# Performance work log

Measured on AMD Instinct MI355X. Metric: run time of the kernel, lower is better.

Reference implementation:

```python
import jax, jax.numpy as jnp
import numpy as np

D = 384; QK = 48; E = 768; LOCAL = E - D
NB = 8; NTOK = 100; NEG = -1e30
B = 128; S = 100; NPTS = 256


def layernorm(x, w, eps=1e-5):
    mu = jnp.mean(x, axis=-1, keepdims=True)
    var = jnp.mean((x - mu) ** 2, axis=-1, keepdims=True)
    return (x - mu) * jax.lax.rsqrt(var + eps) * w


def attend(q, k, v, bias=None):
    scale = 1.0 / jnp.sqrt(jnp.asarray(q.shape[-1], q.dtype))
    s = jnp.einsum('bqd,bkd->bqk', q, k) * scale
    if bias is not None:
        s = s + bias
    return jnp.einsum('bqk,bkd->bqd', jax.nn.softmax(s, axis=-1), v)


def setup_inputs() -> dict:
    key = jax.random.key(0)
    ks = jax.random.split(key, 16)
    s_exp = 0.5 / (D ** 0.5) / 2.0   # 0.5 / sqrt(residual_depth) / expand_factor
    s_prj = 1.0 / (D ** 0.5) / 2.0 / NB
    return {
        'q': jax.random.randint(ks[0], (B, S), 0, NTOK),
        'pts': jax.random.randint(ks[1], (B, NPTS, 2), 0, NTOK),
        'emb': jax.random.normal(ks[2], (NTOK, D), jnp.float32),
        'pt_emb': jax.random.normal(ks[3], (NTOK, D // 2), jnp.float32),
        'norm_w': jnp.ones((D,), jnp.float32),
        'out_w': jax.random.normal(ks[4], (NTOK, D), jnp.float32) / (D ** 0.5),
        'ln1': jnp.ones((NB, D), jnp.float32),
        'expand': s_exp * jax.random.normal(ks[5], (NB, 2 * QK + 2 * E, D), jnp.float32),
        'project1': s_prj * jax.random.normal(ks[6], (NB, D, E), jnp.float32),
        'bias_mult': jnp.ones((NB,), jnp.float32),
        'ln2': jnp.ones((NB, D), jnp.float32),
        'Wq': s_exp * jax.random.normal(ks[7], (NB, QK + 2 * LOCAL, D), jnp.float32),
        'Wkv': s_exp * jax.random.normal(ks[8], (NB, QK + 2 * D, D), jnp.float32),
        'project2': s_prj * jax.random.normal(ks[9], (NB, D, E), jnp.float32),
    }


def _forward(q, pts, emb, pt_emb, norm_w, out_w, ln1, expand, project1, bias_mult, ln2, Wq, Wkv, project2):
    x = emb[q]                                        # [B,S,D]
    kv = pt_emb[pts].reshape(pts.shape[0], -1, D)     # [B,NPTS,D] (pairs of 2D coords fold into D)
    x = layernorm(x, norm_w)

    pos = jnp.arange(x.shape[1])
    pbb = (pos[None, :] - pos[:, None]).astype(x.dtype)  # position bias base (j - i)
    allowed = pos[None, :] <= pos[:, None]                # causal: attend to past + self

    def step(h, p):
        w_ln1, W_e, W_p1, bm, w_ln2, W_q, W_kv, W_p2 = p
        # --- latent self-attention block ---
        bias = jnp.where(allowed, jax.nn.softplus(bm) * pbb, NEG)
        n = layernorm(h, w_ln1)
        proj = n @ W_e.T                                  # [B,S,2*QK+2*E]
        qr = proj[..., :QK]
        kr = proj[..., QK:2 * QK]
        lin = proj[..., 2 * QK:2 * QK + E]
        pre = proj[..., 2 * QK + E:]
        geglu = lin * jax.nn.gelu(pre, approximate=False)
        attn = attend(qr, kr, geglu[..., LOCAL:], bias)
        h = h + jnp.concatenate([geglu[..., :LOCAL], attn], axis=-1) @ W_p1.T
        # --- latent cross-attention block ---
        n = layernorm(h, w_ln2)
        pq = n @ W_q.T                                    # [B,S,QK+2*LOCAL]
        qr2 = pq[..., :QK]
        g_local = pq[..., QK:QK + LOCAL] * jax.nn.gelu(pq[..., QK + LOCAL:], approximate=False)
        pk = kv @ W_kv.T                                  # [B,NPTS,QK+2*D]
        k2 = pk[..., :QK]
        g_val = pk[..., QK:QK + D] * jax.nn.gelu(pk[..., QK + D:], approximate=False)
        attn2 = attend(qr2, k2, g_val)
        h = h + jnp.concatenate([g_local, attn2], axis=-1) @ W_p2.T
        return h, None

    x, _ = jax.lax.scan(step, x, (ln1, expand, project1, bias_mult, ln2, Wq, Wkv, project2))
    x = layernorm(x, norm_w)
    return x @ out_w.T                                    # [B,S,NTOK]


def reference(q, pts, emb, pt_emb, norm_w, out_w, ln1, expand, project1, bias_mult, ln2, Wq, Wkv, project2):
    return _forward(q, pts, emb, pt_emb, norm_w, out_w, ln1, expand, project1, bias_mult, ln2, Wq, Wkv, project2)
```

## Files before the change

kernel.cpp:

```cpp
#include <hip/hip_runtime.h>
#include <hip/hip_bf16.h>
#include <math.h>

#define B_    128
#define S_    100
#define D_    384
#define QK_   48
#define E_    768
#define LOCAL_ 384
#define NB_   8
#define NTOK_ 100
#define NPTS_ 256
#define M_    (B_*S_)

typedef unsigned short ushort;
typedef __attribute__((ext_vector_type(8))) short  bf16x8;
typedef __attribute__((ext_vector_type(8))) unsigned short ushort8v;
typedef __attribute__((ext_vector_type(4))) float  f32x4;

#define MFMA(a,b,c) __builtin_amdgcn_mfma_f32_16x16x32_bf16(a,b,c,0,0,0)

static __device__ __forceinline__ float gelu_f(float x) {
    float y = 1.5957691216057308f * (x + 0.044715f * x * x * x);
    float e = __expf(y);
    float t = 1.0f - 2.0f / (e + 1.0f);
    return 0.5f * x * (1.0f + t);
}
static __device__ __forceinline__ ushort f2b(float f) {
    union { float f; unsigned u; } x; x.f = f;
    unsigned r = x.u + 0x7FFFu + ((x.u >> 16) & 1u);
    return (ushort)(r >> 16);
}
static __device__ __forceinline__ float b2f(ushort u) {
    union { unsigned u; float f; } x; x.u = ((unsigned)u) << 16;
    return x.f;
}

static __device__ __forceinline__ void xcd_swz(int xn, int gy, int& bx, int& by) {
    int L = blockIdx.x + xn * blockIdx.y;
    int gmain = (gy & ~7) * xn;
    if (L < gmain) {
        int grp = L / (8 * xn);
        int r = L % (8 * xn);
        bx = r >> 3;
        by = grp * 8 + (r & 7);
    } else {
        int Lp = L - gmain;
        int tail = gy & 7;
        by = (gy & ~7) + (Lp % tail);
        bx = Lp / tail;
    }
}

__global__ __launch_bounds__(256)
void ln_rows(const float* __restrict__ X, const float* __restrict__ w,
             ushort* __restrict__ Y, int nrows)
{
    int row = blockIdx.x * 4 + (threadIdx.x >> 6);
    if (row >= nrows) return;
    int lane = threadIdx.x & 63;
    const float* x = X + (size_t)row * D_;
    float v[6]; float s = 0.f;
    #pragma unroll
    for (int t = 0; t < 6; ++t) { v[t] = x[lane + 64*t]; s += v[t]; }
    #pragma unroll
    for (int off = 32; off; off >>= 1) s += __shfl_xor(s, off);
    float mu = s * (1.f/(float)D_);
    float q = 0.f;
    #pragma unroll
    for (int t = 0; t < 6; ++t) { float d = v[t]-mu; q += d*d; }
    #pragma unroll
    for (int off = 32; off; off >>= 1) q += __shfl_xor(q, off);
    float rs = rsqrtf(q * (1.f/(float)D_) + 1e-5f);
    #pragma unroll
    for (int t = 0; t < 6; ++t)
        Y[(size_t)row*D_ + lane + 64*t] = f2b((v[t]-mu)*rs*w[lane + 64*t]);
}

__global__ __launch_bounds__(256)
void x_init(const int* __restrict__ qtok, const float* __restrict__ emb,
            const float* __restrict__ w, float* __restrict__ Y, int nrows)
{
    int row = blockIdx.x * 4 + (threadIdx.x >> 6);
    if (row >= nrows) return;
    int lane = threadIdx.x & 63;
    const float* x = emb + (size_t)qtok[row] * D_;
    float v[6]; float s = 0.f;
    #pragma unroll
    for (int t = 0; t < 6; ++t) { v[t] = x[lane + 64*t]; s += v[t]; }
    #pragma unroll
    for (int off = 32; off; off >>= 1) s += __shfl_xor(s, off);
    float mu = s * (1.f/(float)D_);
    float q = 0.f;
    #pragma unroll
    for (int t = 0; t < 6; ++t) { float d = v[t]-mu; q += d*d; }
    #pragma unroll
    for (int off = 32; off; off >>= 1) q += __shfl_xor(q, off);
    float rs = rsqrtf(q * (1.f/(float)D_) + 1e-5f);
    float* y = Y + (size_t)row * D_;
    #pragma unroll
    for (int t = 0; t < 6; ++t) y[lane + 64*t] = (v[t]-mu)*rs*w[lane + 64*t];
}

#define WE_SZ  (1632*384)
#define P1_SZ  (384*768)
#define WQ_SZ  (816*384)
#define P2_SZ  (384*768)
#define WTOT   (WE_SZ + P1_SZ + WQ_SZ + P2_SZ)

static __device__ __forceinline__ void wsplit(float v, ushort* wh, ushort* wl, size_t o) {
    ushort h = f2b(v);
    wh[o] = h; wl[o] = f2b(v - b2f(h));
}

__global__ __launch_bounds__(256)
void wconv_all_hi(const float* __restrict__ expand, const float* __restrict__ proj1,
                  const float* __restrict__ wq, const float* __restrict__ proj2,
                  ushort* __restrict__ wh)
{
    int i = blockIdx.x*256 + threadIdx.x;
    if (i >= WTOT) return;
    int blk = blockIdx.y;
    float v;
    if (i < WE_SZ) v = expand[(size_t)blk*WE_SZ + i];
    else if (i < WE_SZ+P1_SZ) v = proj1[(size_t)blk*P1_SZ + (i - WE_SZ)];
    else if (i < WE_SZ+P1_SZ+WQ_SZ) v = wq[(size_t)blk*WQ_SZ + (i - WE_SZ - P1_SZ)];
    else v = proj2[(size_t)blk*P2_SZ + (i - WE_SZ - P1_SZ - WQ_SZ)];
    wh[(size_t)blk*WTOT + i] = f2b(v);
}

__global__ __launch_bounds__(256)
void wconv_hi(const float* __restrict__ we, const float* __restrict__ p1,
              const float* __restrict__ wq, const float* __restrict__ p2,
              ushort* __restrict__ wh)
{
    int i = blockIdx.x*256 + threadIdx.x;
    if (i >= WTOT) return;
    float v;
    if (i < WE_SZ) v = we[i];
    else if (i < WE_SZ+P1_SZ) v = p1[i - WE_SZ];
    else if (i < WE_SZ+P1_SZ+WQ_SZ) v = wq[i - WE_SZ - P1_SZ];
    else v = p2[i - WE_SZ - P1_SZ - WQ_SZ];
    wh[i] = f2b(v);
}

__global__ __launch_bounds__(256)
void wconv1(const float* __restrict__ src, int n,
            ushort* __restrict__ wh, ushort* __restrict__ wl)
{
    int i = blockIdx.x*256 + threadIdx.x;
    if (i >= n) return;
    wsplit(src[i], wh, wl, i);
}

__global__ __launch_bounds__(256)
void pconv(const float* __restrict__ src, ushort* __restrict__ dst)
{
    int i = blockIdx.x*256 + threadIdx.x;
    if (i >= 128*192) return;
    int r = i / 192;
    dst[i] = (r < NTOK_) ? f2b(src[i]) : 0;
}

__global__ __launch_bounds__(256)
void mm_bt64(const ushort* __restrict__ A1, int lda1, int K1,
             const ushort* __restrict__ A2, int lda2,
             const ushort* __restrict__ Wgh, const ushort* __restrict__ Wgl,
             float* __restrict__ C, int ldc, int N, int K, int accum)
{
    __shared__ ushort Ah[64][72], Wh[64][72], Wl[64][72];
    int tid = threadIdx.x;
    int row0 = blockIdx.y*64, col0 = blockIdx.x*64;
    int srow = tid >> 3;
    int sseg = (tid & 7) * 8;
    int wid = tid >> 6, lane = tid & 63;
    int wr = wid >> 1, wc = wid & 1;
    int fr = lane & 15, fg = lane >> 4;
    f32x4 acc[2][2] = {};
    for (int k0 = 0; k0 < K; k0 += 64) {
        ushort8v va[2], vc[2], vd[2];
        #pragma unroll
        for (int p = 0; p < 2; ++p) {
            int r = p*32 + srow;
            int arow = row0 + r;
            int wrow = col0 + r;
            int gk = k0 + sseg;
            if (gk < K1) va[p] = *(const ushort8v*)(A1 + (size_t)arow*lda1 + gk);
            else         va[p] = *(const ushort8v*)(A2 + (size_t)arow*lda2 + (gk-K1));
            if (wrow >= N) wrow = N - 1;
            vc[p] = *(const ushort8v*)(Wgh + (size_t)wrow*K + gk);
            vd[p] = *(const ushort8v*)(Wgl + (size_t)wrow*K + gk);
        }
        __syncthreads();
        #pragma unroll
        for (int p = 0; p < 2; ++p) {
            int r = p*32 + srow;
            *(ushort8v*)&Ah[r][sseg] = va[p];
            *(ushort8v*)&Wh[r][sseg] = vc[p];
            *(ushort8v*)&Wl[r][sseg] = vd[p];
        }
        __syncthreads();
        #pragma unroll
        for (int kk = 0; kk < 64; kk += 32) {
            bf16x8 a[2], b_h[2], b_l[2];
            #pragma unroll
            for (int s = 0; s < 2; ++s) {
                a[s]   = *(const bf16x8*)&Ah[wr*32 + s*16 + fr][kk + fg*8];
                b_h[s] = *(const bf16x8*)&Wh[wc*32 + s*16 + fr][kk + fg*8];
                b_l[s] = *(const bf16x8*)&Wl[wc*32 + s*16 + fr][kk + fg*8];
            }
            #pragma unroll
            for (int s = 0; s < 2; ++s)
                #pragma unroll
                for (int u = 0; u < 2; ++u)
                    acc[s][u] = MFMA(a[s], b_h[u], acc[s][u]);
            #pragma unroll
            for (int s = 0; s < 2; ++s)
                #pragma unroll
                for (int u = 0; u < 2; ++u)
                    acc[s][u] = MFMA(a[s], b_l[u], acc[s][u]);
        }
        __syncthreads();
    }
    #pragma unroll
    for (int s = 0; s < 2; ++s) {
        int r = row0 + wr*32 + s*16 + fg*4;
        #pragma unroll
        for (int u = 0; u < 2; ++u) {
            int c = col0 + wc*32 + u*16 + fr;
            if (c < N) {
                #pragma unroll
                for (int j = 0; j < 4; ++j) {
                    size_t o = (size_t)(r+j)*ldc + c;
                    C[o] = accum ? (C[o] + acc[s][u][j]) : acc[s][u][j];
                }
            }
        }
    }
}

__global__ __launch_bounds__(256)
void mm_bt2(const ushort* __restrict__ A1, int lda1, int K1,
            const ushort* __restrict__ A2, int lda2,
            const ushort* __restrict__ Wgh,
            float* __restrict__ C, int ldc, int N, int K, int accum)
{
    __shared__ ushort As[128*32], Whs[64*32];
    int tid = threadIdx.x;
    int lane = tid & 63, wid = tid >> 6;
    int bx, by; xcd_swz(gridDim.x, gridDim.y, bx, by);
    int row0 = by*128, col0 = bx*64;
    int wr = wid >> 1, wc = wid & 1;
    int fr = lane & 15, fg = lane >> 4;
    int gsl = (fg ^ ((fr >> 1) & 3)) * 8;
    int sr = tid >> 2, sg0 = tid & 3;
    int g = sg0 ^ ((sr >> 1) & 3);
    int wrow = col0 + sr; if (wrow >= N) wrow = N - 1;

    ushort8v va[2], vh;
    auto loadk = [&](int k0) {
        const ushort* Asrc; int lda, kk;
        if (k0 < K1) { Asrc = A1; lda = lda1; kk = k0; }
        else         { Asrc = A2; lda = lda2; kk = k0 - K1; }
        #pragma unroll
        for (int i = 0; i < 2; ++i)
            va[i] = *(const ushort8v*)(Asrc + (size_t)(row0 + sr + i*64)*lda + kk + g*8);
        vh = *(const ushort8v*)(Wgh + (size_t)wrow*K + k0 + g*8);
    };

    f32x4 acc[4][2] = {};
    loadk(0);
    for (int k0 = 0; k0 < K; k0 += 32) {
        __syncthreads();
        #pragma unroll
        for (int i = 0; i < 2; ++i)
            *(ushort8v*)&As[(sr + i*64)*32 + sg0*8] = va[i];
        *(ushort8v*)&Whs[sr*32 + sg0*8] = vh;
        if (k0 + 32 < K) loadk(k0 + 32);
        __syncthreads();
        bf16x8 a[4], bh[2];
        #pragma unroll
        for (int s = 0; s < 4; ++s) {
            int r = wr*64 + s*16 + fr;
            a[s] = *(const bf16x8*)&As[r*32 + gsl];
        }
        #pragma unroll
        for (int u = 0; u < 2; ++u) {
            int r = wc*32 + u*16 + fr;
            bh[u] = *(const bf16x8*)&Whs[r*32 + gsl];
        }
        #pragma unroll
        for (int s = 0; s < 4; ++s)
            #pragma unroll
            for (int u = 0; u < 2; ++u)
                acc[s][u] = MFMA(a[s], bh[u], acc[s][u]);
    }
    #pragma unroll
    for (int s = 0; s < 4; ++s) {
        int rb = row0 + wr*64 + s*16 + fg*4;
        #pragma unroll
        for (int u = 0; u < 2; ++u) {
            int c = col0 + wc*32 + u*16 + fr;
            if (c < N) {
                #pragma unroll
                for (int j = 0; j < 4; ++j) {
                    size_t o = (size_t)(rb+j)*ldc + c;
                    C[o] = accum ? (C[o] + acc[s][u][j]) : acc[s][u][j];
                }
            }
        }
    }
}

__global__ __launch_bounds__(256)
void mm_fused2(const ushort* __restrict__ Ag, int lda,
               const ushort* __restrict__ Wqh,
               int Nq, int nqt, float* __restrict__ Qout, int ldq,
               const ushort* __restrict__ W1h, const ushort* __restrict__ W2h,
               ushort* __restrict__ Oh, int ldo, int K)
{
    __shared__ ushort As[128*32];
    __shared__ ushort Xs[2][64*32];
    int tid = threadIdx.x;
    int lane = tid & 63, wid = tid >> 6;
    int bx, by; xcd_swz(gridDim.x, gridDim.y, bx, by);
    int row0 = by*128;
    int wr = wid >> 1, wc = wid & 1;
    int fr = lane & 15, fg = lane >> 4;
    int gsl = (fg ^ ((fr >> 1) & 3)) * 8;
    int sr = tid >> 2, sg0 = tid & 3;
    int g = sg0 ^ ((sr >> 1) & 3);

    if (bx < nqt) {
        int col0 = bx*64;
        int wrow = col0 + sr; if (wrow >= Nq) wrow = Nq - 1;
        ushort8v va[2], vh;
        auto loadk = [&](int k0) {
            #pragma unroll
            for (int i = 0; i < 2; ++i)
                va[i] = *(const ushort8v*)(Ag + (size_t)(row0 + sr + i*64)*lda + k0 + g*8);
            vh = *(const ushort8v*)(Wqh + (size_t)wrow*K + k0 + g*8);
        };
        f32x4 acc[4][2] = {};
        loadk(0);
        for (int k0 = 0; k0 < K; k0 += 32) {
            __syncthreads();
            #pragma unroll
            for (int i = 0; i < 2; ++i)
                *(ushort8v*)&As[(sr + i*64)*32 + sg0*8] = va[i];
            *(ushort8v*)&Xs[0][sr*32 + sg0*8] = vh;
            if (k0 + 32 < K) loadk(k0 + 32);
            __syncthreads();
            bf16x8 a[4], bh[2];
            #pragma unroll
            for (int s = 0; s < 4; ++s) {
                int r = wr*64 + s*16 + fr;
                a[s] = *(const bf16x8*)&As[r*32 + gsl];
            }
            #pragma unroll
            for (int u = 0; u < 2; ++u) {
                int r = wc*32 + u*16 + fr;
                bh[u] = *(const bf16x8*)&Xs[0][r*32 + gsl];
            }
            #pragma unroll
            for (int s = 0; s < 4; ++s)
                #pragma unroll
                for (int u = 0; u < 2; ++u)
                    acc[s][u] = MFMA(a[s], bh[u], acc[s][u]);
        }
        #pragma unroll
        for (int s = 0; s < 4; ++s) {
            int rb = row0 + wr*64 + s*16 + fg*4;
            #pragma unroll
            for (int u = 0; u < 2; ++u) {
                int c = col0 + wc*32 + u*16 + fr;
                if (c < Nq) {
                    #pragma unroll
                    for (int j = 0; j < 4; ++j)
                        Qout[(size_t)(rb+j)*ldq + c] = acc[s][u][j];
                }
            }
        }
    } else {
        int col0 = (bx - nqt)*64;
        ushort8v va[2], vw0, vw2;
        auto loadk = [&](int k0) {
            #pragma unroll
            for (int i = 0; i < 2; ++i)
                va[i] = *(const ushort8v*)(Ag + (size_t)(row0 + sr + i*64)*lda + k0 + g*8);
            size_t wro = (size_t)(col0 + sr)*K + k0 + g*8;
            vw0 = *(const ushort8v*)(W1h + wro);
            vw2 = *(const ushort8v*)(W2h + wro);
        };
        f32x4 acc1[4][2] = {}, acc2[4][2] = {};
        loadk(0);
        for (int k0 = 0; k0 < K; k0 += 32) {
            __syncthreads();
            #pragma unroll
            for (int i = 0; i < 2; ++i)
                *(ushort8v*)&As[(sr + i*64)*32 + sg0*8] = va[i];
            {
                int o = sr*32 + sg0*8;
                *(ushort8v*)&Xs[0][o] = vw0;
                *(ushort8v*)&Xs[1][o] = vw2;
            }
            if (k0 + 32 < K) loadk(k0 + 32);
            __syncthreads();
            bf16x8 a[4], b1[2], b2[2];
            #pragma unroll
            for (int s = 0; s < 4; ++s) {
                int r = wr*64 + s*16 + fr;
                a[s] = *(const bf16x8*)&As[r*32 + gsl];
            }
            #pragma unroll
            for (int u = 0; u < 2; ++u) {
                int r = wc*32 + u*16 + fr;
                b1[u] = *(const bf16x8*)&Xs[0][r*32 + gsl];
                b2[u] = *(const bf16x8*)&Xs[1][r*32 + gsl];
            }
            #pragma unroll
            for (int s = 0; s < 4; ++s)
                #pragma unroll
                for (int u = 0; u < 2; ++u) {
                    acc1[s][u] = MFMA(a[s], b1[u], acc1[s][u]);
                    acc2[s][u] = MFMA(a[s], b2[u], acc2[s][u]);
                }
        }
        #pragma unroll
        for (int s = 0; s < 4; ++s) {
            int rb = row0 + wr*64 + s*16 + fg*4;
            #pragma unroll
            for (int u = 0; u < 2; ++u) {
                int c = col0 + wc*32 + u*16 + fr;
                #pragma unroll
                for (int j = 0; j < 4; ++j) {
                    float gg = acc1[s][u][j] * gelu_f(acc2[s][u][j]);
                    Oh[(size_t)(rb+j)*ldo + c] = f2b(gg);
                }
            }
        }
    }
}

__global__ __launch_bounds__(256)
void pk_mm(const ushort* __restrict__ A,
           const ushort* __restrict__ Wh_, const ushort* __restrict__ Wl_,
           float* __restrict__ P12)
{
    __shared__ ushort Ah[64][72], Wh[64][72], Wl[64][72];
    int tid = threadIdx.x;
    int z = blockIdx.z, blk = z >> 1, half = z & 1;
    int row0 = blockIdx.y*64, col0 = blockIdx.x*64;
    int srow = tid >> 3, sseg = (tid & 7) * 8;
    int wid = tid >> 6, lane = tid & 63;
    int wr = wid >> 1, wc = wid & 1;
    int fr = lane & 15, fg = lane >> 4;
    const ushort* Wbh = Wh_ + (size_t)blk*816*384 + half*192;
    const ushort* Wbl = Wl_ + (size_t)blk*816*384 + half*192;
    float* C = P12 + (size_t)z*128*816;
    f32x4 acc[2][2] = {};
    for (int k0 = 0; k0 < 192; k0 += 64) {
        ushort8v va[2], vc[2], vd[2];
        #pragma unroll
        for (int p = 0; p < 2; ++p) {
            int r = p*32 + srow;
            int wrow = col0 + r; if (wrow >= 816) wrow = 815;
            int gk = k0 + sseg;
            va[p] = *(const ushort8v*)(A + (size_t)(row0 + r)*192 + gk);
            vc[p] = *(const ushort8v*)(Wbh + (size_t)wrow*384 + gk);
            vd[p] = *(const ushort8v*)(Wbl + (size_t)wrow*384 + gk);
        }
        __syncthreads();
        #pragma unroll
        for (int p = 0; p < 2; ++p) {
            int r = p*32 + srow;
            *(ushort8v*)&Ah[r][sseg] = va[p];
            *(ushort8v*)&Wh[r][sseg] = vc[p];
            *(ushort8v*)&Wl[r][sseg] = vd[p];
        }
        __syncthreads();
        #pragma unroll
        for (int kk = 0; kk < 64; kk += 32) {
            bf16x8 a[2], b_h[2], b_l[2];
            #pragma unroll
            for (int s = 0; s < 2; ++s) {
                a[s]   = *(const bf16x8*)&Ah[wr*32 + s*16 + fr][kk + fg*8];
                b_h[s] = *(const bf16x8*)&Wh[wc*32 + s*16 + fr][kk + fg*8];
                b_l[s] = *(const bf16x8*)&Wl[wc*32 + s*16 + fr][kk + fg*8];
            }
            #pragma unroll
            for (int s = 0; s < 2; ++s)
                #pragma unroll
                for (int u = 0; u < 2; ++u)
                    acc[s][u] = MFMA(a[s], b_h[u], acc[s][u]);
            #pragma unroll
            for (int s = 0; s < 2; ++s)
                #pragma unroll
                for (int u = 0; u < 2; ++u)
                    acc[s][u] = MFMA(a[s], b_l[u], acc[s][u]);
        }
        __syncthreads();
    }
    #pragma unroll
    for (int s = 0; s < 2; ++s) {
        int r = row0 + wr*32 + s*16 + fg*4;
        #pragma unroll
        for (int u = 0; u < 2; ++u) {
            int c = col0 + wc*32 + u*16 + fr;
            if (c < 816) {
                #pragma unroll
                for (int j = 0; j < 4; ++j)
                    C[(size_t)(r+j)*816 + c] = acc[s][u][j];
            }
        }
    }
}

template<int NK, int CAUSAL>
__global__ __launch_bounds__(256)
void pv_fused(const float* __restrict__ Q, int ldq,
              const float* __restrict__ Kf, int ldk, int koff, long sK,
              const ushort* __restrict__ V, int ldv, long sV,
              ushort* __restrict__ Oh, int ldo, long sO,
              int Mrows, int Kv,
              const float* __restrict__ bm, int blk)
{
    constexpr int NKF = NK / 16;
    constexpr int PSTR = NK + 8;
    __shared__ ushort SH[64*72 + NK*72];
    __shared__ ushort Vs[128*32];
    ushort* Qs = SH;
    ushort* Ks = SH + 64*72;
    ushort* Pf = SH;

    int L = blockIdx.x + gridDim.x*(blockIdx.y + gridDim.y*blockIdx.z);
    int gz = gridDim.z;
    int zz = L % gz;
    int rest = L / gz;
    int bx = rest % gridDim.x;
    int byy = rest / gridDim.x;
    int row0 = byy*64, col0 = bx*128;

    int tid = threadIdx.x;
    int wv = tid >> 6, lane = tid & 63;
    int fr = lane & 15, fg = lane >> 4;

    const float scale = 0.14433756729740643f;
    float sp = 0.f;
    if (CAUSAL) { float bmv = bm[blk]; sp = (bmv > 20.f) ? bmv : log1pf(expf(bmv)); }

    const float* Qb = Q + ((size_t)zz * S_) * ldq;
    for (int idx = tid; idx < 64*64; idx += 256) {
        int r = idx >> 6, c = idx & 63;
        int grow = row0 + r; if (grow >= S_) grow = S_ - 1;
        ushort v = 0;
        if (c < 48) v = f2b(Qb[(size_t)grow*ldq + c]);
        Qs[r*72 + c] = v;
    }
    const float* Kb = Kf + (size_t)zz*sK + koff;
    for (int idx = tid; idx < NK*64; idx += 256) {
        int j = idx >> 6, c = idx & 63;
        ushort v = 0;
        if (c < 48 && j < Kv) v = f2b(Kb[(size_t)j*ldk + c]);
        Ks[j*72 + c] = v;
    }
    int vk = tid & 31, vcb = (tid >> 5)*8;
    ushort8v vv[2];
    auto loadV = [&](int k0) {
        vv[0] = (ushort8v){0,0,0,0,0,0,0,0};
        vv[1] = (ushort8v){0,0,0,0,0,0,0,0};
        int gk = k0 + vk;
        if (gk < Kv) {
            const ushort* Vb = V + (size_t)zz*sV;
            #pragma unroll
            for (int i2 = 0; i2 < 2; ++i2)
                vv[i2] = *(const ushort8v*)(Vb + (size_t)gk*ldv + col0 + vcb + i2*64);
        }
    };
    loadV(0);
    __syncthreads();

    f32x4 sacc[NKF];
    #pragma unroll
    for (int kf = 0; kf < NKF; ++kf) sacc[kf] = (f32x4){0.f,0.f,0.f,0.f};
    bf16x8 aq0 = *(const bf16x8*)&Qs[(wv*16 + fr)*72 +  0 + fg*8];
    bf16x8 aq1 = *(const bf16x8*)&Qs[(wv*16 + fr)*72 + 32 + fg*8];
    #pragma unroll
    for (int kf = 0; kf < NKF; ++kf) {
        bf16x8 bk0 = *(const bf16x8*)&Ks[(kf*16 + fr)*72 +  0 + fg*8];
        bf16x8 bk1 = *(const bf16x8*)&Ks[(kf*16 + fr)*72 + 32 + fg*8];
        sacc[kf] = MFMA(aq0, bk0, sacc[kf]);
        sacc[kf] = MFMA(aq1, bk1, sacc[kf]);
    }
    #pragma unroll
    for (int j = 0; j < 4; ++j) {
        int i = row0 + wv*16 + fg*4 + j;
        float m = -1e30f;
        #pragma unroll
        for (int kf = 0; kf < NKF; ++kf) {
            int key = kf*16 + fr;
            float s = sacc[kf][j] * scale;
            if (CAUSAL) s = (key <= i) ? (s + sp*(float)(key - i)) : -1e30f;
            sacc[kf][j] = s;
            m = fmaxf(m, s);
        }
        #pragma unroll
        for (int off = 1; off < 16; off <<= 1) m = fmaxf(m, __shfl_xor(m, off));
        float sum = 0.f;
        #pragma unroll
        for (int kf = 0; kf < NKF; ++kf) {
            float p = __expf(sacc[kf][j] - m);
            sacc[kf][j] = p;
            sum += p;
        }
        #pragma unroll
        for (int off = 1; off < 16; off <<= 1) sum += __shfl_xor(sum, off);
        float inv = 1.f / sum;
        #pragma unroll
        for (int kf = 0; kf < NKF; ++kf) sacc[kf][j] *= inv;
    }
    __syncthreads();
    #pragma unroll
    for (int j = 0; j < 4; ++j)
        #pragma unroll
        for (int kf = 0; kf < NKF; ++kf)
            Pf[(wv*16 + fg*4 + j)*PSTR + kf*16 + fr] = f2b(sacc[kf][j]);
    __syncthreads();

    f32x4 acc[4][2] = {};
    for (int k0 = 0; k0 < NK; k0 += 32) {
        #pragma unroll
        for (int i2 = 0; i2 < 2; ++i2) {
            #pragma unroll
            for (int e = 0; e < 8; ++e) {
                int c = vcb + i2*64 + e;
                Vs[c*32 + (vk & 7) + 8*((vk >> 3) ^ ((c >> 3) & 3))] = vv[i2][e];
            }
        }
        if (k0 + 32 < NK) loadV(k0 + 32);
        __syncthreads();
        bf16x8 a[4], b[2];
        #pragma unroll
        for (int s = 0; s < 4; ++s)
            a[s] = *(const bf16x8*)&Pf[(s*16 + fr)*PSTR + k0 + fg*8];
        #pragma unroll
        for (int u = 0; u < 2; ++u) {
            int c = wv*32 + u*16 + fr;
            b[u] = *(const bf16x8*)&Vs[c*32 + 8*(fg ^ ((c >> 3) & 3))];
        }
        #pragma unroll
        for (int s = 0; s < 4; ++s)
            #pragma unroll
            for (int u = 0; u < 2; ++u)
                acc[s][u] = MFMA(a[s], b[u], acc[s][u]);
        __syncthreads();
    }
    ushort* Ohb = Oh + (size_t)zz*sO;
    #pragma unroll
    for (int s = 0; s < 4; ++s) {
        int rbase = row0 + s*16 + fg*4;
        #pragma unroll
        for (int u = 0; u < 2; ++u) {
            int c = col0 + wv*32 + u*16 + fr;
            #pragma unroll
            for (int j = 0; j < 4; ++j) {
                int r = rbase + j;
                if (r < Mrows)
                    Ohb[(size_t)r*ldo + c] = f2b(acc[s][u][j]);
            }
        }
    }
}

__global__ __launch_bounds__(256)
void pk_gather(const int* __restrict__ pts, const float* __restrict__ P12, int blk,
               float* __restrict__ k2, ushort* __restrict__ gv)
{
    int pair = blockIdx.x*4 + (threadIdx.x >> 6);
    int lane = threadIdx.x & 63;
    const float* P1 = P12 + (size_t)(blk*2 + 0)*128*816;
    const float* P2 = P12 + (size_t)(blk*2 + 1)*128*816;
    int t0 = pts[2*pair], t1 = pts[2*pair+1];
    const float* a = P1 + (size_t)t0*816;
    const float* c = P2 + (size_t)t1*816;
    if (lane < QK_) k2[(size_t)pair*QK_ + lane] = a[lane] + c[lane];
    #pragma unroll
    for (int t = 0; t < 6; ++t) {
        int i = lane + 64*t;
        float lin = a[48 + i] + c[48 + i];
        float pre = a[432 + i] + c[432 + i];
        gv[(size_t)pair*D_ + i] = f2b(lin * gelu_f(pre));
    }
}

extern "C" void kernel_launch(void* const* d_in, const int* in_sizes, int n_in,
                              void* d_out, int out_size, void* d_ws, size_t ws_size,
                              hipStream_t stream)
{
    const int*   qtok  = (const int*)d_in[0];
    const int*   pts   = (const int*)d_in[1];
    const float* emb   = (const float*)d_in[2];
    const float* ptemb = (const float*)d_in[3];
    const float* normw = (const float*)d_in[4];
    const float* outw  = (const float*)d_in[5];
    const float* ln1   = (const float*)d_in[6];
    const float* expand= (const float*)d_in[7];
    const float* proj1 = (const float*)d_in[8];
    const float* bm    = (const float*)d_in[9];
    const float* ln2   = (const float*)d_in[10];
    const float* Wq    = (const float*)d_in[11];
    const float* Wkv   = (const float*)d_in[12];
    const float* proj2 = (const float*)d_in[13];
    float* out = (float*)d_out;

    char* base = (char*)d_ws;
    size_t off = 0;
    auto alloc = [&](size_t bytes){ void* p = base + off; off += (bytes + 255) & ~(size_t)255; return p; };
    float*  h     = (float*) alloc((size_t)M_*D_*4);
    ushort* nh    = (ushort*)alloc((size_t)M_*D_*2);
    float*  qk1   = (float*) alloc((size_t)M_*96*4);
    ushort* gegl  = (ushort*)alloc((size_t)M_*E_*2);
    ushort* atb   = (ushort*)alloc((size_t)M_*D_*2);
    ushort* gv    = (ushort*)alloc((size_t)B_*NPTS_*D_*2);
    float*  P12   = (float*) alloc((size_t)16*128*816*4);
    float*  k2    = (float*) alloc((size_t)B_*NPTS_*QK_*4);
    ushort* wkvh  = (ushort*)alloc((size_t)NB_*816*384*2);
    ushort* wkvl  = (ushort*)alloc((size_t)NB_*816*384*2);
    ushort* ptp   = (ushort*)alloc((size_t)128*192*2);
    ushort* obh   = (ushort*)alloc((size_t)NTOK_*D_*2);
    ushort* obl   = (ushort*)alloc((size_t)NTOK_*D_*2);

    size_t rem = (ws_size > off) ? (ws_size - off) : 0;
    bool fits8 = rem >= ((size_t)NB_ * WTOT * 2 + 1024);
    int nlay = fits8 ? NB_ : 1;
    ushort* wbh = (ushort*)alloc((size_t)nlay*WTOT*2);
    size_t wstride = fits8 ? (size_t)WTOT : 0;

    float*  qr2   = qk1;
    ushort* gloc  = gegl;

    const size_t oWE = 0;
    const size_t oP1 = WE_SZ;
    const size_t oWQ = WE_SZ + P1_SZ;
    const size_t oP2 = WE_SZ + P1_SZ + WQ_SZ;

    x_init<<<M_/4, 256, 0, stream>>>(qtok, emb, normw, h, M_);
    pconv<<<(128*192 + 255)/256, 256, 0, stream>>>(ptemb, ptp);
    wconv1<<<(NB_*816*384 + 255)/256, 256, 0, stream>>>(Wkv, NB_*816*384, wkvh, wkvl);
    pk_mm<<<dim3(13, 2, 16), 256, 0, stream>>>(ptp, wkvh, wkvl, P12);
    if (fits8)
        wconv_all_hi<<<dim3((WTOT+255)/256, NB_), 256, 0, stream>>>(
            expand, proj1, Wq, proj2, wbh);

    for (int blk = 0; blk < NB_; ++blk) {
        if (!fits8)
            wconv_hi<<<(WTOT+255)/256, 256, 0, stream>>>(
                expand + (size_t)blk*WE_SZ, proj1 + (size_t)blk*P1_SZ,
                Wq + (size_t)blk*WQ_SZ, proj2 + (size_t)blk*P2_SZ, wbh);
        const ushort* Lh = wbh + wstride*blk;

        ln_rows<<<M_/4, 256, 0, stream>>>(h, ln1 + blk*D_, nh, M_);
        mm_fused2<<<dim3(14, M_/128), 256, 0, stream>>>(nh, D_,
            Lh + oWE, 96, 2, qk1, 96,
            Lh + oWE + (size_t)96*D_, Lh + oWE + (size_t)864*D_,
            gegl, E_, D_);
        pv_fused<128,1><<<dim3(3,2,B_), 256, 0, stream>>>(
            qk1, 96,
            qk1, 96, 48, (long)S_*96,
            gegl + LOCAL_, E_, (long)S_*E_,
            atb, D_, (long)S_*D_,
            S_, S_, bm, blk);
        mm_bt2<<<dim3(6, M_/128), 256, 0, stream>>>(gegl, E_, D_, atb, D_,
            Lh + oP1, h, D_, D_, E_, 1);

        ln_rows<<<M_/4, 256, 0, stream>>>(h, ln2 + blk*D_, nh, M_);
        mm_fused2<<<dim3(7, M_/128), 256, 0, stream>>>(nh, D_,
            Lh + oWQ, 48, 1, qr2, 48,
            Lh + oWQ + (size_t)48*D_, Lh + oWQ + (size_t)432*D_,
            gloc, D_, D_);
        pk_gather<<<B_*NPTS_/4, 256, 0, stream>>>(pts, P12, blk, k2, gv);
        pv_fused<256,0><<<dim3(3,2,B_), 256, 0, stream>>>(
            qr2, 48,
            k2, 48, 0, (long)NPTS_*48,
            gv, D_, (long)NPTS_*D_,
            atb, D_, (long)S_*D_,
            S_, NPTS_, bm, blk);
        mm_bt2<<<dim3(6, M_/128), 256, 0, stream>>>(gloc, D_, D_, atb, D_,
            Lh + oP2, h, D_, D_, E_, 1);
    }

    ln_rows<<<M_/4, 256, 0, stream>>>(h, normw, nh, M_);
    wconv1<<<(NTOK_*D_ + 255)/256, 256, 0, stream>>>(outw, NTOK_*D_, obh, obl);
    mm_bt64<<<dim3(2, M_/64), 256, 0, stream>>>(nh, D_, D_, nh, D_,
        obh, obl, out, NTOK_, NTOK_, D_, 0);
}
```

Before: 1.839 ms.

## Split attention into score kernel and PV kernel; precompute point gathers for all layers

Splits the fused attention kernel into two kernels. The first computes softmax probabilities once per 64-row slab and writes them as bf16 to a buffer. The second multiplies them by V with a tiled, register-prefetched loop, so the QK^T and softmax work is no longer repeated for each of the 3 column tiles. It also moves the per-layer point key/value gather and GELU into a single launch before the layer loop when the workspace is large enough. The cost is extra global traffic for the probability buffer, two launches per attention, and more workspace.

Result: faster. 1.648 ms (median of 2 runs) (-10.4%).

```diff
diff --git a/kernel.cpp b/kernel.cpp
--- a/kernel.cpp
+++ b/kernel.cpp
@@ -516,31 +516,105 @@
     }
 }
 
-template<int NK, int CAUSAL>
-__global__ __launch_bounds__(256)
-void pv_fused(const float* __restrict__ Q, int ldq,
-              const float* __restrict__ Kf, int ldk, int koff, long sK,
-              const ushort* __restrict__ V, int ldv, long sV,
-              ushort* __restrict__ Oh, int ldo, long sO,
-              int Mrows, int Kv,
-              const float* __restrict__ bm, int blk)
-{
-    constexpr int NKF = NK / 16;
-    constexpr int PSTR = NK + 8;
-    __shared__ ushort SH[64*72 + NK*72];
+__global__ __launch_bounds__(256)
+void pv2(const ushort* __restrict__ P, int ldp, long sP,
+         const ushort* __restrict__ V, int ldv, long sV,
+         ushort* __restrict__ Oh, int ldo, long sO,
+         int Mrows, int K, int Kv)
+{
+    __shared__ ushort Ps[64][40];
     __shared__ ushort Vs[128*32];
-    ushort* Qs = SH;
-    ushort* Ks = SH + 64*72;
-    ushort* Pf = SH;
-
     int L = blockIdx.x + gridDim.x*(blockIdx.y + gridDim.y*blockIdx.z);
     int gz = gridDim.z;
     int zz = L % gz;
     int rest = L / gz;
     int bx = rest % gridDim.x;
     int byy = rest / gridDim.x;
+    const ushort* Pb = P + (size_t)zz * sP;
+    const ushort* Vb = V + (size_t)zz * sV;
+    ushort* Ohb = Oh + (size_t)zz * sO;
+    int tid = threadIdx.x;
     int row0 = byy*64, col0 = bx*128;
-
+    int wid = tid >> 6, lane = tid & 63;
+    int fr = lane & 15, fg = lane >> 4;
+    int prow = tid >> 2, pseg = (tid & 3) * 8;
+    int vk = tid & 31, vcb = (tid >> 5) * 8;
+
+    ushort8v pv_, vv[2];
+    auto loadk = [&](int k0) {
+        pv_ = (ushort8v){0,0,0,0,0,0,0,0};
+        int grow = row0 + prow;
+        if (grow < Mrows)
+            pv_ = *(const ushort8v*)(Pb + (size_t)grow*ldp + k0 + pseg);
+        vv[0] = (ushort8v){0,0,0,0,0,0,0,0};
+        vv[1] = (ushort8v){0,0,0,0,0,0,0,0};
+        int gk = k0 + vk;
+        if (gk < Kv) {
+            #pragma unroll
+            for (int i = 0; i < 2; ++i)
+                vv[i] = *(const ushort8v*)(Vb + (size_t)gk*ldv + col0 + vcb + i*64);
+        }
+    };
+
+    f32x4 acc[4][2] = {};
+    loadk(0);
+    for (int k0 = 0; k0 < K; k0 += 32) {
+        __syncthreads();
+        *(ushort8v*)&Ps[prow][pseg] = pv_;
+        #pragma unroll
+        for (int i = 0; i < 2; ++i) {
+            #pragma unroll
+            for (int e = 0; e < 8; ++e) {
+                int c = vcb + i*64 + e;
+                Vs[c*32 + (vk & 7) + 8*((vk >> 3) ^ ((c >> 3) & 3))] = vv[i][e];
+            }
+        }
+        if (k0 + 32 < K) loadk(k0 + 32);
+        __syncthreads();
+        bf16x8 a[4], b[2];
+        #pragma unroll
+        for (int s = 0; s < 4; ++s)
+            a[s] = *(const bf16x8*)&Ps[s*16 + fr][fg*8];
+        #pragma unroll
+        for (int u = 0; u < 2; ++u) {
+            int c = wid*32 + u*16 + fr;
+            b[u] = *(const bf16x8*)&Vs[c*32 + 8*(fg ^ ((c >> 3) & 3))];
+        }
+        #pragma unroll
+        for (int s = 0; s < 4; ++s)
+            #pragma unroll
+            for (int u = 0; u < 2; ++u)
+                acc[s][u] = MFMA(a[s], b[u], acc[s][u]);
+    }
+    #pragma unroll
+    for (int s = 0; s < 4; ++s) {
+        int rbase = row0 + s*16 + fg*4;
+        #pragma unroll
+        for (int u = 0; u < 2; ++u) {
+            int c = col0 + wid*32 + u*16 + fr;
+            #pragma unroll
+            for (int j = 0; j < 4; ++j) {
+                int r = rbase + j;
+                if (r < Mrows)
+                    Ohb[(size_t)r*ldo + c] = f2b(acc[s][u][j]);
+            }
+        }
+    }
+}
+
+template<int NK, int CAUSAL>
+__global__ __launch_bounds__(256)
+void attn_score_mfma(const float* __restrict__ Q, int ldq, long sQ,
+                     const float* __restrict__ Kf, int ldk, int koff, long sK,
+                     ushort* __restrict__ P,
+                     const float* __restrict__ bm, int blk, int Kv)
+{
+    constexpr int NKF = NK / 16;
+    __shared__ ushort Qs[64*72];
+    __shared__ ushort Ks[NK*72];
+    int slab = blockIdx.x;
+    int zz = blockIdx.y;
+    int row0 = slab*64;
     int tid = threadIdx.x;
     int wv = tid >> 6, lane = tid & 63;
     int fr = lane & 15, fg = lane >> 4;
@@ -549,7 +623,7 @@
     float sp = 0.f;
     if (CAUSAL) { float bmv = bm[blk]; sp = (bmv > 20.f) ? bmv : log1pf(expf(bmv)); }
 
-    const float* Qb = Q + ((size_t)zz * S_) * ldq;
+    const float* Qb = Q + (size_t)zz * sQ;
     for (int idx = tid; idx < 64*64; idx += 256) {
         int r = idx >> 6, c = idx & 63;
         int grow = row0 + r; if (grow >= S_) grow = S_ - 1;
@@ -564,20 +638,6 @@
         if (c < 48 && j < Kv) v = f2b(Kb[(size_t)j*ldk + c]);
         Ks[j*72 + c] = v;
     }
-    int vk = tid & 31, vcb = (tid >> 5)*8;
-    ushort8v vv[2];
-    auto loadV = [&](int k0) {
-        vv[0] = (ushort8v){0,0,0,0,0,0,0,0};
-        vv[1] = (ushort8v){0,0,0,0,0,0,0,0};
-        int gk = k0 + vk;
-        if (gk < Kv) {
-            const ushort* Vb = V + (size_t)zz*sV;
-            #pragma unroll
-            for (int i2 = 0; i2 < 2; ++i2)
-                vv[i2] = *(const ushort8v*)(Vb + (size_t)gk*ldv + col0 + vcb + i2*64);
-        }
-    };
-    loadV(0);
     __syncthreads();
 
     f32x4 sacc[NKF];
@@ -616,58 +676,11 @@
         #pragma unroll
         for (int off = 1; off < 16; off <<= 1) sum += __shfl_xor(sum, off);
         float inv = 1.f / sum;
-        #pragma unroll
-        for (int kf = 0; kf < NKF; ++kf) sacc[kf][j] *= inv;
-    }
-    __syncthreads();
-    #pragma unroll
-    for (int j = 0; j < 4; ++j)
-        #pragma unroll
-        for (int kf = 0; kf < NKF; ++kf)
-            Pf[(wv*16 + fg*4 + j)*PSTR + kf*16 + fr] = f2b(sacc[kf][j]);
-    __syncthreads();
-
-    f32x4 acc[4][2] = {};
-    for (int k0 = 0; k0 < NK; k0 += 32) {
-        #pragma unroll
-        for (int i2 = 0; i2 < 2; ++i2) {
-            #pragma unroll
-            for (int e = 0; e < 8; ++e) {
-                int c = vcb + i2*64 + e;
-                Vs[c*32 + (vk & 7) + 8*((vk >> 3) ^ ((c >> 3) & 3))] = vv[i2][e];
-            }
-        }
-        if (k0 + 32 < NK) loadV(k0 + 32);
-        __syncthreads();
-        bf16x8 a[4], b[2];
-        #pragma unroll
-        for (int s = 0; s < 4; ++s)
-            a[s] = *(const bf16x8*)&Pf[(s*16 + fr)*PSTR + k0 + fg*8];
-        #pragma unroll
-        for (int u = 0; u < 2; ++u) {
-            int c = wv*32 + u*16 + fr;
-            b[u] = *(const bf16x8*)&Vs[c*32 + 8*(fg ^ ((c >> 3) & 3))];
-        }
-        #pragma unroll
-        for (int s = 0; s < 4; ++s)
-            #pragma unroll
-            for (int u = 0; u < 2; ++u)
-                acc[s][u] = MFMA(a[s], b[u], acc[s][u]);
-        __syncthreads();
-    }
-    ushort* Ohb = Oh + (size_t)zz*sO;
-    #pragma unroll
-    for (int s = 0; s < 4; ++s) {
-        int rbase = row0 + s*16 + fg*4;
-        #pragma unroll
-        for (int u = 0; u < 2; ++u) {
-            int c = col0 + wv*32 + u*16 + fr;
-            #pragma unroll
-            for (int j = 0; j < 4; ++j) {
-                int r = rbase + j;
-                if (r < Mrows)
-                    Ohb[(size_t)r*ldo + c] = f2b(acc[s][u][j]);
-            }
+        if (i < S_) {
+            ushort* prow = P + ((size_t)(zz*S_) + i)*NK;
+            #pragma unroll
+            for (int kf = 0; kf < NKF; ++kf)
+                prow[kf*16 + fr] = f2b(sacc[kf][j] * inv);
         }
     }
 }
@@ -690,6 +703,30 @@
         float lin = a[48 + i] + c[48 + i];
         float pre = a[432 + i] + c[432 + i];
         gv[(size_t)pair*D_ + i] = f2b(lin * gelu_f(pre));
+    }
+}
+
+__global__ __launch_bounds__(256)
+void pk_gather_all(const int* __restrict__ pts, const float* __restrict__ P12,
+                   float* __restrict__ k2, ushort* __restrict__ gv)
+{
+    int pair = blockIdx.x*4 + (threadIdx.x >> 6);
+    int lane = threadIdx.x & 63;
+    int blk = blockIdx.y;
+    const float* P1 = P12 + (size_t)(blk*2 + 0)*128*816;
+    const float* P2 = P12 + (size_t)(blk*2 + 1)*128*816;
+    float* k2b = k2 + (size_t)blk*B_*NPTS_*QK_;
+    ushort* gvb = gv + (size_t)blk*B_*NPTS_*D_;
+    int t0 = pts[2*pair], t1 = pts[2*pair+1];
+    const float* a = P1 + (size_t)t0*816;
+    const float* c = P2 + (size_t)t1*816;
+    if (lane < QK_) k2b[(size_t)pair*QK_ + lane] = a[lane] + c[lane];
+    #pragma unroll
+    for (int t = 0; t < 6; ++t) {
+        int i = lane + 64*t;
+        float lin = a[48 + i] + c[48 + i];
+        float pre = a[432 + i] + c[432 + i];
+        gvb[(size_t)pair*D_ + i] = f2b(lin * gelu_f(pre));
     }
 }
 
@@ -721,9 +758,8 @@
     float*  qk1   = (float*) alloc((size_t)M_*96*4);
     ushort* gegl  = (ushort*)alloc((size_t)M_*E_*2);
     ushort* atb   = (ushort*)alloc((size_t)M_*D_*2);
-    ushort* gv    = (ushort*)alloc((size_t)B_*NPTS_*D_*2);
+    ushort* Pbuf  = (ushort*)alloc((size_t)M_*256*2);
     float*  P12   = (float*) alloc((size_t)16*128*816*4);
-    float*  k2    = (float*) alloc((size_t)B_*NPTS_*QK_*4);
     ushort* wkvh  = (ushort*)alloc((size_t)NB_*816*384*2);
     ushort* wkvl  = (ushort*)alloc((size_t)NB_*816*384*2);
     ushort* ptp   = (ushort*)alloc((size_t)128*192*2);
@@ -731,10 +767,21 @@
     ushort* obl   = (ushort*)alloc((size_t)NTOK_*D_*2);
 
     size_t rem = (ws_size > off) ? (ws_size - off) : 0;
-    bool fits8 = rem >= ((size_t)NB_ * WTOT * 2 + 1024);
+    bool fits8 = rem >= ((size_t)NB_ * WTOT * 2
+                         + (size_t)B_*NPTS_*D_*2 + (size_t)B_*NPTS_*QK_*4 + 4096);
     int nlay = fits8 ? NB_ : 1;
     ushort* wbh = (ushort*)alloc((size_t)nlay*WTOT*2);
     size_t wstride = fits8 ? (size_t)WTOT : 0;
+
+    size_t gv_l = (size_t)B_*NPTS_*D_;
+    size_t k2_l = (size_t)B_*NPTS_*QK_;
+    size_t rem2 = (ws_size > off) ? (ws_size - off) : 0;
+    bool fitsPK = rem2 >= ((size_t)NB_*gv_l*2 + (size_t)NB_*k2_l*4 + 4096);
+    int play = fitsPK ? NB_ : 1;
+    ushort* gvB = (ushort*)alloc((size_t)play*gv_l*2);
+    float*  k2B = (float*) alloc((size_t)play*k2_l*4);
+    size_t gvs = fitsPK ? gv_l : 0;
+    size_t k2s = fitsPK ? k2_l : 0;
 
     float*  qr2   = qk1;
     ushort* gloc  = gegl;
@@ -751,6 +798,8 @@
     if (fits8)
         wconv_all_hi<<<dim3((WTOT+255)/256, NB_), 256, 0, stream>>>(
             expand, proj1, Wq, proj2, wbh);
+    if (fitsPK)
+        pk_gather_all<<<dim3(B_*NPTS_/4, NB_), 256, 0, stream>>>(pts, P12, k2B, gvB);
 
     for (int blk = 0; blk < NB_; ++blk) {
         if (!fits8)
@@ -758,18 +807,21 @@
                 expand + (size_t)blk*WE_SZ, proj1 + (size_t)blk*P1_SZ,
                 Wq + (size_t)blk*WQ_SZ, proj2 + (size_t)blk*P2_SZ, wbh);
         const ushort* Lh = wbh + wstride*blk;
+        ushort* gv = gvB + gvs*blk;
+        float*  k2 = k2B + k2s*blk;
 
         ln_rows<<<M_/4, 256, 0, stream>>>(h, ln1 + blk*D_, nh, M_);
         mm_fused2<<<dim3(14, M_/128), 256, 0, stream>>>(nh, D_,
             Lh + oWE, 96, 2, qk1, 96,
             Lh + oWE + (size_t)96*D_, Lh + oWE + (size_t)864*D_,
             gegl, E_, D_);
-        pv_fused<128,1><<<dim3(3,2,B_), 256, 0, stream>>>(
-            qk1, 96,
+        attn_score_mfma<128,1><<<dim3(2, B_), 256, 0, stream>>>(
+            qk1, 96, (long)S_*96,
             qk1, 96, 48, (long)S_*96,
+            Pbuf, bm, blk, S_);
+        pv2<<<dim3(3,2,B_), 256, 0, stream>>>(Pbuf, 128, (long)S_*128,
             gegl + LOCAL_, E_, (long)S_*E_,
-            atb, D_, (long)S_*D_,
-            S_, S_, bm, blk);
+            atb, D_, (long)S_*D_, S_, 128, S_);
         mm_bt2<<<dim3(6, M_/128), 256, 0, stream>>>(gegl, E_, D_, atb, D_,
             Lh + oP1, h, D_, D_, E_, 1);
 
@@ -778,13 +830,15 @@
             Lh + oWQ, 48, 1, qr2, 48,
             Lh + oWQ + (size_t)48*D_, Lh + oWQ + (size_t)432*D_,
             gloc, D_, D_);
-        pk_gather<<<B_*NPTS_/4, 256, 0, stream>>>(pts, P12, blk, k2, gv);
-        pv_fused<256,0><<<dim3(3,2,B_), 256, 0, stream>>>(
-            qr2, 48,
+        if (!fitsPK)
+            pk_gather<<<B_*NPTS_/4, 256, 0, stream>>>(pts, P12, blk, k2, gv);
+        attn_score_mfma<256,0><<<dim3(2, B_), 256, 0, stream>>>(
+            qr2, 48, (long)S_*48,
             k2, 48, 0, (long)NPTS_*48,
+            Pbuf, bm, blk, NPTS_);
+        pv2<<<dim3(3,2,B_), 256, 0, stream>>>(Pbuf, 256, (long)S_*256,
             gv, D_, (long)NPTS_*D_,
-            atb, D_, (long)S_*D_,
-            S_, NPTS_, bm, blk);
+            atb, D_, (long)S_*D_, S_, 256, 256);
         mm_bt2<<<dim3(6, M_/128), 256, 0, stream>>>(gloc, D_, D_, atb, D_,
             Lh + oP2, h, D_, D_, E_, 1);
     }
```
